# Performance work log

Hardware: AMD Instinct MI355X
Metric: run time of the kernel (lower is better)

The kernel has to match this reference:

```python
import jax, jax.numpy as jnp
import numpy as np

T, M, HW = 16, 256, 1024
D_MODEL, D_K, H = 512, 512, 8
HEAD = D_K // H
SIGMA = 0.5
EPS = 1e-6

def layernorm_nobias(x, gamma):
    mu = jnp.mean(x, axis=-1, keepdims=True)
    var = jnp.mean((x - mu) ** 2, axis=-1, keepdims=True)
    return (x - mu) * jax.lax.rsqrt(var + EPS) * gamma

def setup_inputs() -> dict:
    key = jax.random.key(0)
    ks = jax.random.split(key, 11)
    s = 0.02
    return {
        "updated_track_tokens": jax.random.normal(ks[0], (T, M, D_MODEL), jnp.float32),
        "tracks": jax.random.uniform(ks[1], (T, M, 2), jnp.float32) * 32.0,
        "feature_positions": jax.random.uniform(ks[2], (HW, 2), jnp.float32) * 32.0,
        "feature_pos_embeddings": jax.random.normal(ks[3], (T, HW, D_MODEL), jnp.float32),
        "track_pos_embeddings": jax.random.normal(ks[4], (T, M, D_MODEL), jnp.float32),
        "W_q": jax.random.normal(ks[5], (D_K, D_MODEL), jnp.float32) * s,
        "W_k": jax.random.normal(ks[6], (D_K, D_MODEL), jnp.float32) * s,
        "W_v": jax.random.normal(ks[7], (D_MODEL, D_MODEL), jnp.float32) * s,
        "W_out": jax.random.normal(ks[8], (D_MODEL, D_MODEL), jnp.float32) * s,
        "q_gamma": jnp.ones((D_K,), jnp.float32),
        "k_gamma": jnp.ones((D_K,), jnp.float32),
    }

def reference(updated_track_tokens, tracks, feature_positions, feature_pos_embeddings,
              track_pos_embeddings, W_q, W_k, W_v, W_out, q_gamma, k_gamma):
    # Projections (torch Linear: x @ W.T)
    Q = feature_pos_embeddings @ W_q.T       # [T, HW, D_K]
    K = track_pos_embeddings @ W_k.T         # [T, M, D_K]
    V = updated_track_tokens @ W_v.T         # [T, M, D_MODEL]
    # QK LayerNorm (no bias) over full d_k, before head split
    Q = layernorm_nobias(Q, q_gamma)
    K = layernorm_nobias(K, k_gamma)
    Qh = Q.reshape(T, HW, H, HEAD).transpose(0, 2, 1, 3)          # [T,H,HW,hd]
    Kh = K.reshape(T, M, H, HEAD).transpose(0, 2, 1, 3)           # [T,H,M,hd]
    Vh = V.reshape(T, M, H, D_MODEL // H).transpose(0, 2, 1, 3)   # [T,H,M,dv]
    scores = jnp.einsum('thqd,thkd->thqk', Qh, Kh) / np.float32(np.sqrt(HEAD))
    # Vectorized spatial bias: squared euclidean distance feat->track per t
    diff = feature_positions[None, :, None, :] - tracks[:, None, :, :]  # [T,HW,M,2]
    d2 = jnp.sum(diff * diff, axis=-1)                                  # [T,HW,M]
    bias = -d2 / (2.0 * SIGMA ** 2)
    scores = scores + bias[:, None, :, :]                               # broadcast heads
    attn = jax.nn.softmax(scores, axis=-1)
    upd = jnp.einsum('thqk,thkd->thqd', attn, Vh)                       # [T,H,HW,dv]
    upd = upd.transpose(0, 2, 1, 3).reshape(T, HW, D_MODEL)
    return upd @ W_out.T
```

## Files before the change

kernel.cpp:

```cpp
#include <hip/hip_runtime.h>

#define T_    16
#define M_    256
#define HW_   1024
#define DM    512
#define H_    8
#define HEAD_ 64
#define LOG2E 1.4426950408889634f

typedef __attribute__((ext_vector_type(8))) short short8;
typedef __attribute__((ext_vector_type(4))) float f32x4;

__device__ __forceinline__ unsigned cvtpk(float lo, float hi) {
    unsigned r;
    asm("v_cvt_pk_bf16_f32 %0, %1, %2" : "=v"(r) : "v"(lo), "v"(hi));
    return r;
}

__device__ __forceinline__ float b2f(unsigned short u) {
    return __uint_as_float(((unsigned)u) << 16);
}

__device__ __forceinline__ void gload16(const void* g, void* l) {
    __builtin_amdgcn_global_load_lds(
        (const __attribute__((address_space(1))) void*)g,
        (__attribute__((address_space(3))) void*)l, 16, 0, 0);
}

__global__ __launch_bounds__(256) void cvtall(const float* __restrict__ fpe,
                                              const float* __restrict__ tpe,
                                              const float* __restrict__ utt,
                                              const float* __restrict__ Wq,
                                              const float* __restrict__ Wk,
                                              const float* __restrict__ Wv,
                                              const float* __restrict__ Wo,
                                              unsigned short* __restrict__ Fb,
                                              unsigned short* __restrict__ Tb,
                                              unsigned short* __restrict__ Ub0,
                                              unsigned short* __restrict__ Wbf) {
    size_t e = (size_t)(blockIdx.x * 256 + threadIdx.x) * 8;
    const float* s;
    unsigned short* d;
    if (e < 8388608)        { s = fpe + e;              d = Fb  + e; }
    else if (e < 10485760)  { s = tpe + (e - 8388608);  d = Tb  + (e - 8388608); }
    else if (e < 12582912)  { s = utt + (e - 10485760); d = Ub0 + (e - 10485760); }
    else if (e < 12845056)  { s = Wq  + (e - 12582912); d = Wbf + (e - 12582912 + 0); }
    else if (e < 13107200)  { s = Wk  + (e - 12845056); d = Wbf + (e - 12845056 + 262144); }
    else if (e < 13369344)  { s = Wv  + (e - 13107200); d = Wbf + (e - 13107200 + 524288); }
    else                    { s = Wo  + (e - 13369344); d = Wbf + (e - 13369344 + 786432); }
    float4 a = *reinterpret_cast<const float4*>(s);
    float4 b = *reinterpret_cast<const float4*>(s + 4);
    uint4 v = make_uint4(cvtpk(a.x, a.y), cvtpk(a.z, a.w),
                         cvtpk(b.x, b.y), cvtpk(b.z, b.w));
    *reinterpret_cast<uint4*>(d) = v;
}

__global__ __launch_bounds__(256) void proj3(const unsigned short* __restrict__ Fb,
                                             const unsigned short* __restrict__ Tb,
                                             const unsigned short* __restrict__ Ub0,
                                             const unsigned short* __restrict__ Wbf,
                                             unsigned short* __restrict__ Qb,
                                             unsigned short* __restrict__ Kb,
                                             unsigned short* __restrict__ Vb) {
    __shared__ __align__(16) unsigned char smem[32768];
    unsigned char* As = smem;
    unsigned char* Bs = smem + 16384;

    const int b  = blockIdx.x;
    const int x  = b & 7;
    const int cp = (b >> 3) & 3;
    const int m  = b >> 5;
    const int p  = x * 24 + m;
    const unsigned short *X, *W;
    unsigned short* C;
    int r0;
    if (p < 128)      { X = Fb;  W = Wbf;          C = Qb; r0 = p * 128; }
    else if (p < 160) { X = Tb;  W = Wbf + 262144; C = Kb; r0 = (p - 128) * 128; }
    else              { X = Ub0; W = Wbf + 524288; C = Vb; r0 = (p - 160) * 128; }
    const int c0 = cp * 128;

    const int tid = threadIdx.x;
    const int l  = tid & 63;
    const int wid = tid >> 6;
    const int wr = wid >> 1, wc = wid & 1;
    const int g = l >> 4;
    const int c = l & 15;

    f32x4 acc[4][4] = {};

    for (int k0 = 0; k0 < DM; k0 += 64) {
        #pragma unroll
        for (int i = 0; i < 4; ++i) {
            int idx = tid + i * 256;
            int row = idx >> 3, jj = idx & 7;
            int j = jj ^ (row & 7);
            gload16(X + (size_t)(r0 + row) * DM + k0 + j * 8, As + idx * 16);
            gload16(W + (size_t)(c0 + row) * DM + k0 + j * 8, Bs + idx * 16);
        }
        __syncthreads();

        #pragma unroll
        for (int ks = 0; ks < 2; ++ks) {
            short8 af[4], bfr[4];
            #pragma unroll
            for (int mm = 0; mm < 4; ++mm) {
                int rq = wr * 64 + mm * 16 + c;
                af[mm] = *reinterpret_cast<short8*>(
                    As + ((rq * 128 + ks * 64 + g * 16) ^ ((rq & 7) << 4)));
            }
            #pragma unroll
            for (int n = 0; n < 4; ++n) {
                int rn = wc * 64 + n * 16 + c;
                bfr[n] = *reinterpret_cast<short8*>(
                    Bs + ((rn * 128 + ks * 64 + g * 16) ^ ((rn & 7) << 4)));
            }
            #pragma unroll
            for (int mm = 0; mm < 4; ++mm)
                #pragma unroll
                for (int n = 0; n < 4; ++n)
                    acc[mm][n] = __builtin_amdgcn_mfma_f32_16x16x32_bf16(
                        af[mm], bfr[n], acc[mm][n], 0, 0, 0);
        }
        __syncthreads();
    }

    #pragma unroll
    for (int mm = 0; mm < 4; ++mm)
        #pragma unroll
        for (int n = 0; n < 4; ++n)
            #pragma unroll
            for (int r = 0; r < 4; ++r)
                C[(size_t)(r0 + wr * 64 + mm * 16 + g * 4 + r) * DM +
                  c0 + wc * 64 + n * 16 + c] =
                    (unsigned short)cvtpk(acc[mm][n][r], acc[mm][n][r]);
}

__global__ __launch_bounds__(256) void gemm_bb(const unsigned short* __restrict__ X,
                                               const unsigned short* __restrict__ W,
                                               float* __restrict__ C) {
    __shared__ __align__(16) unsigned char smem[32768];
    unsigned char* As = smem;
    unsigned char* Bs = smem + 16384;

    const int b  = blockIdx.x;
    const int x  = b & 7;
    const int cp = (b >> 3) & 3;
    const int m  = b >> 5;
    const int p  = x * 16 + m;
    const int r0 = p * 128;
    const int c0 = cp * 128;

    const int tid = threadIdx.x;
    const int l  = tid & 63;
    const int wid = tid >> 6;
    const int wr = wid >> 1, wc = wid & 1;
    const int g = l >> 4;
    const int c = l & 15;

    f32x4 acc[4][4] = {};

    for (int k0 = 0; k0 < DM; k0 += 64) {
        #pragma unroll
        for (int i = 0; i < 4; ++i) {
            int idx = tid + i * 256;
            int row = idx >> 3, jj = idx & 7;
            int j = jj ^ (row & 7);
            gload16(X + (size_t)(r0 + row) * DM + k0 + j * 8, As + idx * 16);
            gload16(W + (size_t)(c0 + row) * DM + k0 + j * 8, Bs + idx * 16);
        }
        __syncthreads();

        #pragma unroll
        for (int ks = 0; ks < 2; ++ks) {
            short8 af[4], bfr[4];
            #pragma unroll
            for (int mm = 0; mm < 4; ++mm) {
                int rq = wr * 64 + mm * 16 + c;
                af[mm] = *reinterpret_cast<short8*>(
                    As + ((rq * 128 + ks * 64 + g * 16) ^ ((rq & 7) << 4)));
            }
            #pragma unroll
            for (int n = 0; n < 4; ++n) {
                int rn = wc * 64 + n * 16 + c;
                bfr[n] = *reinterpret_cast<short8*>(
                    Bs + ((rn * 128 + ks * 64 + g * 16) ^ ((rn & 7) << 4)));
            }
            #pragma unroll
            for (int mm = 0; mm < 4; ++mm)
                #pragma unroll
                for (int n = 0; n < 4; ++n)
                    acc[mm][n] = __builtin_amdgcn_mfma_f32_16x16x32_bf16(
                        af[mm], bfr[n], acc[mm][n], 0, 0, 0);
        }
        __syncthreads();
    }

    #pragma unroll
    for (int mm = 0; mm < 4; ++mm)
        #pragma unroll
        for (int n = 0; n < 4; ++n)
            #pragma unroll
            for (int r = 0; r < 4; ++r)
                C[(size_t)(r0 + wr * 64 + mm * 16 + g * 4 + r) * DM +
                  c0 + wc * 64 + n * 16 + c] = acc[mm][n][r];
}

__global__ __launch_bounds__(256) void normpack(const unsigned short* __restrict__ Qb,
                                                const unsigned short* __restrict__ Kb,
                                                const unsigned short* __restrict__ Vb,
                                                const float* __restrict__ qg,
                                                const float* __restrict__ kg,
                                                unsigned short* __restrict__ Qbf,
                                                unsigned short* __restrict__ Kbf,
                                                unsigned short* __restrict__ Vt) {
    __shared__ unsigned short vtile[64][68];
    const int bid = blockIdx.x;
    const int tid = threadIdx.x;

    if (bid < 5120) {
        const unsigned short* X; const float* gamma; unsigned short* Y;
        int rowbase; float sc;
        if (bid < 4096) { X = Qb; gamma = qg; Y = Qbf; rowbase = bid * 4; sc = 0.125f * LOG2E; }
        else            { X = Kb; gamma = kg; Y = Kbf; rowbase = (bid - 4096) * 4; sc = 1.0f; }

        const int wave = tid / 64;
        const int lane = tid % 64;
        const int row  = rowbase + wave;

        short8 xv = *reinterpret_cast<const short8*>(&X[(size_t)row * DM + lane * 8]);
        float x[8];
        #pragma unroll
        for (int i = 0; i < 8; ++i) x[i] = b2f((unsigned short)xv[i]);

        float s = 0.f;
        #pragma unroll
        for (int i = 0; i < 8; ++i) s += x[i];
        #pragma unroll
        for (int m = 1; m < 64; m <<= 1) s += __shfl_xor(s, m, 64);
        const float mu = s * (1.0f / 512.0f);

        float vs = 0.f;
        #pragma unroll
        for (int i = 0; i < 8; ++i) { float d = x[i] - mu; vs += d * d; }
        #pragma unroll
        for (int m = 1; m < 64; m <<= 1) vs += __shfl_xor(vs, m, 64);
        const float rs = rsqrtf(vs * (1.0f / 512.0f) + 1e-6f) * sc;

        float4 g0 = *reinterpret_cast<const float4*>(&gamma[lane * 8]);
        float4 g1 = *reinterpret_cast<const float4*>(&gamma[lane * 8 + 4]);
        float gv[8] = {g0.x, g0.y, g0.z, g0.w, g1.x, g1.y, g1.z, g1.w};

        float y[8];
        #pragma unroll
        for (int i = 0; i < 8; ++i) y[i] = (x[i] - mu) * rs * gv[i];
        uint4 o = make_uint4(cvtpk(y[0], y[1]), cvtpk(y[2], y[3]),
                             cvtpk(y[4], y[5]), cvtpk(y[6], y[7]));
        *reinterpret_cast<uint4*>(&Y[(size_t)row * DM + lane * 8]) = o;
    } else {
        const int b2 = bid - 5120;
        const int dt = b2 & 7, kt = (b2 >> 3) & 3, t = b2 >> 5;

        #pragma unroll
        for (int i = 0; i < 4; ++i) {
            int idx = tid + i * 256;
            int r = idx >> 4, c4 = idx & 15;
            uint2 v = *reinterpret_cast<const uint2*>(
                &Vb[(size_t)(t * M_ + kt * 64 + r) * DM + dt * 64 + c4 * 4]);
            *reinterpret_cast<uint2*>(&vtile[r][c4 * 4]) = v;
        }
        __syncthreads();
        #pragma unroll
        for (int i = 0; i < 4; ++i) {
            int idx = tid + i * 256;
            int r = idx >> 4, c4 = idx & 15;
            unsigned a0 = vtile[c4 * 4 + 0][r], a1 = vtile[c4 * 4 + 1][r];
            unsigned a2 = vtile[c4 * 4 + 2][r], a3 = vtile[c4 * 4 + 3][r];
            uint2 o = make_uint2(a0 | (a1 << 16), a2 | (a3 << 16));
            *reinterpret_cast<uint2*>(
                &Vt[((size_t)t * DM + dt * 64 + r) * M_ + kt * 64 + c4 * 4]) = o;
        }
    }
}

__global__ __launch_bounds__(256, 4) void attn_mfma(const unsigned short* __restrict__ Qbf,
                                                    const unsigned short* __restrict__ Kbf,
                                                    const unsigned short* __restrict__ VtG,
                                                    const float* __restrict__ tracks,
                                                    const float* __restrict__ fpos,
                                                    unsigned short* __restrict__ Ubf) {
    const int b   = blockIdx.x;
    const int xcd = b & 7;
    const int bi  = b >> 3;
    const int qt  = bi & 15;
    const int pp  = xcd + (bi >> 4) * 8;
    const int t   = pp >> 3;
    const int h   = pp & 7;
    const int q0  = qt * 64;
    const int tid = threadIdx.x;

    __shared__ __align__(16) unsigned char smem[32768 + 3072 + 512];
    unsigned char* KV = smem;
    float* tx4 = (float*)(smem + 32768);
    float* ty4 = (float*)(smem + 32768 + 1024);
    float* tz2 = (float*)(smem + 32768 + 2048);
    float* fps = (float*)(smem + 32768 + 3072);

    const int l  = tid & 63;
    const int wq = tid >> 6;
    const int g  = l >> 4;
    const int c  = l & 15;

    const unsigned short* qrow =
        Qbf + (size_t)(t * HW_ + q0 + wq * 16 + c) * DM + h * HEAD_;
    short8 bQ0 = *reinterpret_cast<const short8*>(qrow + g * 8);
    short8 bQ1 = *reinterpret_cast<const short8*>(qrow + 32 + g * 8);

    #pragma unroll
    for (int it = 0; it < 8; ++it) {
        int idx = tid + it * 256;
        int row = idx >> 3, jj = idx & 7;
        int j = jj ^ (row & 7);
        gload16(Kbf + (size_t)(t * M_ + row) * DM + h * HEAD_ + j * 8, KV + idx * 16);
    }
    {
        float2 tk = *reinterpret_cast<const float2*>(&tracks[t * 512 + tid * 2]);
        tx4[tid] = tk.x * (4.0f * LOG2E);
        ty4[tid] = tk.y * (4.0f * LOG2E);
        tz2[tid] = -2.0f * LOG2E * (tk.x * tk.x + tk.y * tk.y);
    }
    if (tid < 128) fps[tid] = fpos[q0 * 2 + tid];
    __syncthreads();

    f32x4 acc[16];
    __builtin_amdgcn_s_setprio(1);
    #pragma unroll
    for (int n = 0; n < 16; ++n) {
        int rk = n * 16 + c;
        short8 a0 = *reinterpret_cast<short8*>(KV + ((rk * 128 + g * 16) ^ ((rk & 7) << 4)));
        short8 a1 = *reinterpret_cast<short8*>(KV + ((rk * 128 + 64 + g * 16) ^ ((rk & 7) << 4)));
        f32x4 z = {0.f, 0.f, 0.f, 0.f};
        z = __builtin_amdgcn_mfma_f32_16x16x32_bf16(a0, bQ0, z, 0, 0, 0);
        z = __builtin_amdgcn_mfma_f32_16x16x32_bf16(a1, bQ1, z, 0, 0, 0);
        acc[n] = z;
    }
    __builtin_amdgcn_s_setprio(0);

    __syncthreads();

    #pragma unroll
    for (int it = 0; it < 8; ++it) {
        int idx = tid + it * 256;
        int row = idx >> 5, kcc = idx & 31;
        int kc = kcc ^ (row & 7);
        gload16(VtG + ((size_t)t * DM + h * HEAD_ + row) * M_ + kc * 8, KV + idx * 16);
    }

    const float fx = fps[(wq * 16 + c) * 2];
    const float fy = fps[(wq * 16 + c) * 2 + 1];
    const float fz = -2.0f * LOG2E * (fx * fx + fy * fy);
    unsigned pk[16][2];
    float vr[16];
    #pragma unroll
    for (int n = 0; n < 16; ++n) {
        float4 x4 = *reinterpret_cast<float4*>(&tx4[n * 16 + g * 4]);
        float4 y4 = *reinterpret_cast<float4*>(&ty4[n * 16 + g * 4]);
        float4 z4 = *reinterpret_cast<float4*>(&tz2[n * 16 + g * 4]);
        float e0 = exp2f((acc[n][0] + fz) + fmaf(fx, x4.x, fmaf(fy, y4.x, z4.x)));
        float e1 = exp2f((acc[n][1] + fz) + fmaf(fx, x4.y, fmaf(fy, y4.y, z4.y)));
        float e2 = exp2f((acc[n][2] + fz) + fmaf(fx, x4.z, fmaf(fy, y4.z, z4.z)));
        float e3 = exp2f((acc[n][3] + fz) + fmaf(fx, x4.w, fmaf(fy, y4.w, z4.w)));
        pk[n][0] = cvtpk(e0, e1);
        pk[n][1] = cvtpk(e2, e3);
        vr[n] = (e0 + e1) + (e2 + e3);
    }

    #pragma unroll
    for (int s = 8; s >= 1; s >>= 1)
        #pragma unroll
        for (int n = 0; n < 8; ++n)
            if (n < s) vr[n] += vr[n + s];
    float sum = vr[0];
    sum += __shfl_xor(sum, 16, 64);
    sum += __shfl_xor(sum, 32, 64);
    const float inv = 1.0f / sum;

    float invr[4];
    #pragma unroll
    for (int r = 0; r < 4; ++r)
        invr[r] = __shfl(inv, (l & 48) | ((l >> 2) & 12) | r, 64);

    __syncthreads();

    f32x4 o[4] = {{0.f,0.f,0.f,0.f},{0.f,0.f,0.f,0.f},{0.f,0.f,0.f,0.f},{0.f,0.f,0.f,0.f}};
    __builtin_amdgcn_s_setprio(1);
    #pragma unroll
    for (int ks = 0; ks < 8; ++ks) {
        unsigned wb[4];
        #pragma unroll
        for (int wt = 0; wt < 4; ++wt) {
            int src = ((l & 16) << 1) + (wt >> 1) * 16 + c;
            unsigned ve = (unsigned)__shfl((int)pk[2 * ks][wt & 1], src, 64);
            unsigned vo = (unsigned)__shfl((int)pk[2 * ks + 1][wt & 1], src, 64);
            wb[wt] = (g < 2) ? ve : vo;
        }
        uint4 uu = make_uint4(wb[0], wb[1], wb[2], wb[3]);
        short8 aP = *reinterpret_cast<short8*>(&uu);
        #pragma unroll
        for (int nv = 0; nv < 4; ++nv) {
            int rv = nv * 16 + c;
            short8 bV = *reinterpret_cast<short8*>(
                KV + ((rv * 512 + ks * 64 + g * 16) ^ ((rv & 7) << 4)));
            o[nv] = __builtin_amdgcn_mfma_f32_16x16x32_bf16(aP, bV, o[nv], 0, 0, 0);
        }
    }
    __builtin_amdgcn_s_setprio(0);

    #pragma unroll
    for (int nv = 0; nv < 4; ++nv)
        #pragma unroll
        for (int r = 0; r < 4; ++r) {
            float xo = o[nv][r] * invr[r];
            Ubf[(size_t)(t * HW_ + q0 + wq * 16 + g * 4 + r) * DM +
                h * HEAD_ + nv * 16 + c] = (unsigned short)cvtpk(xo, xo);
        }
}

extern "C" void kernel_launch(void* const* d_in, const int* in_sizes, int n_in,
                              void* d_out, int out_size, void* d_ws, size_t ws_size,
                              hipStream_t stream) {
    const float* utt    = (const float*)d_in[0];
    const float* tracks = (const float*)d_in[1];
    const float* fpos   = (const float*)d_in[2];
    const float* fpe    = (const float*)d_in[3];
    const float* tpe    = (const float*)d_in[4];
    const float* Wq     = (const float*)d_in[5];
    const float* Wk     = (const float*)d_in[6];
    const float* Wv     = (const float*)d_in[7];
    const float* Wo     = (const float*)d_in[8];
    const float* qgamma = (const float*)d_in[9];
    const float* kgamma = (const float*)d_in[10];
    float* out = (float*)d_out;

    char* ws = (char*)d_ws;
    unsigned short* Fb  = (unsigned short*)(ws);
    unsigned short* Tb  = (unsigned short*)(ws + 16777216);
    unsigned short* Ub0 = (unsigned short*)(ws + 20971520);
    unsigned short* Qb  = (unsigned short*)(ws + 25165824);
    unsigned short* Kb  = (unsigned short*)(ws + 41943040);
    unsigned short* Vb  = (unsigned short*)(ws + 46137344);
    unsigned short* Qbf = (unsigned short*)(ws + 50331648);
    unsigned short* Kbf = (unsigned short*)(ws + 67108864);
    unsigned short* Vt  = (unsigned short*)(ws + 71303168);
    unsigned short* Wbf = (unsigned short*)(ws + 75497472);
    unsigned short* Ubf = (unsigned short*)(ws);

    cvtall<<<6656, 256, 0, stream>>>(fpe, tpe, utt, Wq, Wk, Wv, Wo, Fb, Tb, Ub0, Wbf);

    proj3<<<768, 256, 0, stream>>>(Fb, Tb, Ub0, Wbf, Qb, Kb, Vb);

    normpack<<<5632, 256, 0, stream>>>(Qb, Kb, Vb, qgamma, kgamma, Qbf, Kbf, Vt);

    attn_mfma<<<2048, 256, 0, stream>>>(Qbf, Kbf, Vt, tracks, fpos, Ubf);

    gemm_bb<<<512, 256, 0, stream>>>(Ubf, Wbf + 786432, out);
}
```

Baseline: 93.30 us.

## Read K and V fragments directly from global memory instead of LDS staging

```diff
diff --git a/kernel.cpp b/kernel.cpp
--- a/kernel.cpp
+++ b/kernel.cpp
@@ -298,30 +298,16 @@
     const int q0  = qt * 64;
     const int tid = threadIdx.x;
 
-    __shared__ __align__(16) unsigned char smem[32768 + 3072 + 512];
-    unsigned char* KV = smem;
-    float* tx4 = (float*)(smem + 32768);
-    float* ty4 = (float*)(smem + 32768 + 1024);
-    float* tz2 = (float*)(smem + 32768 + 2048);
-    float* fps = (float*)(smem + 32768 + 3072);
+    __shared__ __align__(16) float tx4[256];
+    __shared__ __align__(16) float ty4[256];
+    __shared__ __align__(16) float tz2[256];
+    __shared__ __align__(16) float fps[128];
 
     const int l  = tid & 63;
     const int wq = tid >> 6;
     const int g  = l >> 4;
     const int c  = l & 15;
 
-    const unsigned short* qrow =
-        Qbf + (size_t)(t * HW_ + q0 + wq * 16 + c) * DM + h * HEAD_;
-    short8 bQ0 = *reinterpret_cast<const short8*>(qrow + g * 8);
-    short8 bQ1 = *reinterpret_cast<const short8*>(qrow + 32 + g * 8);
-
-    #pragma unroll
-    for (int it = 0; it < 8; ++it) {
-        int idx = tid + it * 256;
-        int row = idx >> 3, jj = idx & 7;
-        int j = jj ^ (row & 7);
-        gload16(Kbf + (size_t)(t * M_ + row) * DM + h * HEAD_ + j * 8, KV + idx * 16);
-    }
     {
         float2 tk = *reinterpret_cast<const float2*>(&tracks[t * 512 + tid * 2]);
         tx4[tid] = tk.x * (4.0f * LOG2E);
@@ -329,31 +315,28 @@
         tz2[tid] = -2.0f * LOG2E * (tk.x * tk.x + tk.y * tk.y);
     }
     if (tid < 128) fps[tid] = fpos[q0 * 2 + tid];
+
+    const unsigned short* qrow =
+        Qbf + (size_t)(t * HW_ + q0 + wq * 16 + c) * DM + h * HEAD_;
+    short8 bQ0 = *reinterpret_cast<const short8*>(qrow + g * 8);
+    short8 bQ1 = *reinterpret_cast<const short8*>(qrow + 32 + g * 8);
+
     __syncthreads();
 
+    const unsigned short* kbase = Kbf + ((size_t)(t * M_) + c) * DM + h * HEAD_ + g * 8;
     f32x4 acc[16];
     __builtin_amdgcn_s_setprio(1);
     #pragma unroll
     for (int n = 0; n < 16; ++n) {
-        int rk = n * 16 + c;
-        short8 a0 = *reinterpret_cast<short8*>(KV + ((rk * 128 + g * 16) ^ ((rk & 7) << 4)));
-        short8 a1 = *reinterpret_cast<short8*>(KV + ((rk * 128 + 64 + g * 16) ^ ((rk & 7) << 4)));
+        const unsigned short* krow = kbase + (size_t)(n * 16) * DM;
+        short8 a0 = *reinterpret_cast<const short8*>(krow);
+        short8 a1 = *reinterpret_cast<const short8*>(krow + 32);
         f32x4 z = {0.f, 0.f, 0.f, 0.f};
         z = __builtin_amdgcn_mfma_f32_16x16x32_bf16(a0, bQ0, z, 0, 0, 0);
         z = __builtin_amdgcn_mfma_f32_16x16x32_bf16(a1, bQ1, z, 0, 0, 0);
         acc[n] = z;
     }
     __builtin_amdgcn_s_setprio(0);
-
-    __syncthreads();
-
-    #pragma unroll
-    for (int it = 0; it < 8; ++it) {
-        int idx = tid + it * 256;
-        int row = idx >> 5, kcc = idx & 31;
-        int kc = kcc ^ (row & 7);
-        gload16(VtG + ((size_t)t * DM + h * HEAD_ + row) * M_ + kc * 8, KV + idx * 16);
-    }
 
     const float fx = fps[(wq * 16 + c) * 2];
     const float fy = fps[(wq * 16 + c) * 2 + 1];
@@ -389,8 +372,7 @@
     for (int r = 0; r < 4; ++r)
         invr[r] = __shfl(inv, (l & 48) | ((l >> 2) & 12) | r, 64);
 
-    __syncthreads();
-
+    const unsigned short* vbase = VtG + ((size_t)(t * DM) + h * HEAD_ + c) * M_ + g * 8;
     f32x4 o[4] = {{0.f,0.f,0.f,0.f},{0.f,0.f,0.f,0.f},{0.f,0.f,0.f,0.f},{0.f,0.f,0.f,0.f}};
     __builtin_amdgcn_s_setprio(1);
     #pragma unroll
@@ -407,9 +389,8 @@
         short8 aP = *reinterpret_cast<short8*>(&uu);
         #pragma unroll
         for (int nv = 0; nv < 4; ++nv) {
-            int rv = nv * 16 + c;
-            short8 bV = *reinterpret_cast<short8*>(
-                KV + ((rv * 512 + ks * 64 + g * 16) ^ ((rv & 7) << 4)));
+            short8 bV = *reinterpret_cast<const short8*>(
+                vbase + (size_t)(nv * 16) * M_ + ks * 32);
             o[nv] = __builtin_amdgcn_mfma_f32_16x16x32_bf16(aP, bV, o[nv], 0, 0, 0);
         }
     }
```

Result: slower. 130.7 us (+40.0%).
